# Performance work log

Measured on AMD Instinct MI355X. Metric: run time of the kernel, lower is better.

## Reference

```python
import jax, jax.numpy as jnp
import numpy as np

N_NODES = 100000
N_EDGES = 1600000
D_IN = 64
D_HID = 64
D_OUT = 64


def setup_inputs() -> dict:
    key = jax.random.key(0)
    ks = jax.random.split(key, 12)
    x = jax.random.normal(ks[0], (N_NODES, D_IN), dtype=jnp.float32)
    edge_index = jax.random.randint(ks[1], (2, N_EDGES), 0, N_NODES, dtype=jnp.int64)
    batch = jnp.zeros((N_NODES,), dtype=jnp.int64)
    # Glorot-ish init for GCNConv weights; PyG stores weight as [in, out] applied as x @ W.
    def lin(k, din, dout):
        s = 1.0 / np.sqrt(din)
        return jax.random.uniform(k, (din, dout), minval=-s, maxval=s, dtype=jnp.float32)
    W1 = lin(ks[2], D_IN, D_HID);  b1 = jnp.zeros((D_HID,), jnp.float32)
    W2 = lin(ks[3], D_HID, D_HID); b2 = jnp.zeros((D_HID,), jnp.float32)
    W3 = lin(ks[4], D_HID, D_HID); b3 = jnp.zeros((D_HID,), jnp.float32)
    W4 = lin(ks[5], D_HID, D_OUT); b4 = jnp.zeros((D_OUT,), jnp.float32)
    return {"x": x, "edge_index": edge_index, "batch": batch,
            "W1": W1, "b1": b1, "W2": W2, "b2": b2,
            "W3": W3, "b3": b3, "W4": W4, "b4": b4}


def reference(x, edge_index, batch, W1, b1, W2, b2, W3, b3, W4, b4):
    N = x.shape[0]
    loops = jnp.arange(N, dtype=edge_index.dtype)
    src = jnp.concatenate([edge_index[0], loops])  # [E+N]
    dst = jnp.concatenate([edge_index[1], loops])  # [E+N]
    # Symmetric normalization: deg over A + I (in-degree at dst), norm_e = d_src^-1/2 * d_dst^-1/2
    deg = jax.ops.segment_sum(jnp.ones(src.shape, dtype=x.dtype), dst, num_segments=N)
    dis = jnp.where(deg > 0, jax.lax.rsqrt(deg), 0.0)
    norm = (dis[src] * dis[dst])[:, None]  # [E+N, 1]

    def conv(h, W, b):
        h = h @ W                                   # [N, dout]
        msg = h[src] * norm                         # gather + scale, [E+N, dout]
        return jax.ops.segment_sum(msg, dst, num_segments=N) + b

    h = jax.nn.elu(conv(x, W1, b1))   # dropout_p=0.0 -> identity
    h = jax.nn.elu(conv(h, W2, b2))
    h = jax.nn.elu(conv(h, W3, b3))
    return conv(h, W4, b4)
```

## Files before the change

### kernel.cpp

```cpp
#include <hip/hip_runtime.h>

#define NN 100000
#define NE 1600000
#define DD 64
#define BSH 9
#define BSZ 512
#define NBKT 196
#define BCAP 16384
#define CHUNK 8192
#define NCH ((NE + CHUNK - 1) / CHUNK)
#define CSR2_CAP (NE + 16 * NN + 1024)


__global__ void k_zero(int* __restrict__ bcur, int* __restrict__ gcur,
                       float* __restrict__ h2sA, float* __restrict__ h2sB) {
    int t = threadIdx.x;
    if (t < NBKT) bcur[t] = 0;
    if (t == 255) *gcur = 0;
    if (t < DD) h2sA[(size_t)NN * DD + t] = 0.f;
    if (t >= 64 && t < 128) h2sB[(size_t)NN * DD + (t - 64)] = 0.f;
}


__global__ __launch_bounds__(256) void k_bscat(const int* __restrict__ ei,
                                               int* __restrict__ bcur,
                                               int* __restrict__ bkt) {
    __shared__ int h[NBKT], rbase[NBKT], rcur[NBKT];
    int t = threadIdx.x;
    for (int i = t; i < NBKT; i += 256) h[i] = 0;
    __syncthreads();
    int cb = blockIdx.x * CHUNK;
    int s[32], d[32];
#pragma unroll
    for (int i = 0; i < 32; ++i) {
        int e = cb + t + 256 * i;
        if (e < NE) {
            s[i] = ei[e];
            d[i] = ei[NE + e];
            atomicAdd(&h[d[i] >> BSH], 1);
        } else {
            d[i] = -1;
        }
    }
    __syncthreads();
    for (int i = t; i < NBKT; i += 256) {
        int c = h[i];
        rbase[i] = c ? atomicAdd(&bcur[i], c) : 0;
        rcur[i] = 0;
    }
    __syncthreads();
#pragma unroll
    for (int i = 0; i < 32; ++i) {
        if (d[i] >= 0) {
            int b = d[i] >> BSH;
            int pos = rbase[b] + atomicAdd(&rcur[b], 1);
            bkt[(size_t)b * BCAP + pos] = s[i] | ((d[i] & (BSZ - 1)) << 17);
        }
    }
}


__global__ __launch_bounds__(256) void k_merge(const int* __restrict__ bcur,
                                               const int* __restrict__ bkt,
                                               int* __restrict__ gcur,
                                               int* __restrict__ rbeg,
                                               int* __restrict__ rlen,
                                               double* __restrict__ dis,
                                               int* __restrict__ csr2) {
    __shared__ int cnt[BSZ];
    __shared__ int cur[BSZ];
    __shared__ int s2[256];
    __shared__ int sbase;
    int b = blockIdx.x, t = threadIdx.x;
    cnt[t] = 0; cnt[t + 256] = 0;
    __syncthreads();
    int ec = bcur[b];
    const int* row = bkt + (size_t)b * BCAP;
    for (int j = t; j < ec; j += 256)
        atomicAdd(&cnt[row[j] >> 17], 1);
    __syncthreads();
    int nb = b * BSZ;
    int n0 = nb + 2 * t, n1 = nb + 2 * t + 1;
    int c0 = (n0 < NN) ? cnt[2 * t] : -1;
    int c1 = (n1 < NN) ? cnt[2 * t + 1] : -1;
    int q0 = (c0 >= 0) ? ((c0 + 16) & ~15) : 0;
    int q1 = (c1 >= 0) ? ((c1 + 16) & ~15) : 0;
    s2[t] = q0 + q1;
    __syncthreads();
    for (int o = 1; o < 256; o <<= 1) {
        int v = (t >= o) ? s2[t - o] : 0;
        __syncthreads();
        s2[t] += v;
        __syncthreads();
    }
    if (t == 255) sbase = atomicAdd(gcur, s2[255]);
    __syncthreads();
    int base = sbase;
    int ex = s2[t] - (q0 + q1);
    if (c0 >= 0) {
        rbeg[n0] = base + ex; rlen[n0] = q0;
        dis[n0] = 1.0 / sqrt((double)(c0 + 1));
        csr2[base + ex] = n0;
        cur[2 * t] = ex + 1;
    }
    if (c1 >= 0) {
        rbeg[n1] = base + ex + q0; rlen[n1] = q1;
        dis[n1] = 1.0 / sqrt((double)(c1 + 1));
        csr2[base + ex + q0] = n1;
        cur[2 * t + 1] = ex + q0 + 1;
    }
    __syncthreads();
    for (int j = t; j < ec; j += 256) {
        int pk = row[j];
        int pos = base + atomicAdd(&cur[pk >> 17], 1);
        csr2[pos] = pk & 0x1FFFF;
    }
    __syncthreads();
    if (c0 >= 0) { int e0 = ex + q0;      for (int j = cur[2 * t];     j < e0; ++j) csr2[base + j] = NN; }
    if (c1 >= 0) { int e1 = ex + q0 + q1; for (int j = cur[2 * t + 1]; j < e1; ++j) csr2[base + j] = NN; }
}


__global__ __launch_bounds__(256) void k_gemm(const float* __restrict__ in,
                                              const float* __restrict__ W,
                                              const double* __restrict__ dis,
                                              float* __restrict__ h2s) {
    __shared__ float sW[DD * DD];
    __shared__ float sIn[128 * 65];
    int t = threadIdx.x;
    int brow = blockIdx.x * 128;
#pragma unroll
    for (int i = 0; i < 16; ++i) sW[t + 256 * i] = W[t + 256 * i];
#pragma unroll
    for (int i = 0; i < 32; ++i) {
        int idx = t + 256 * i;
        int rr = idx >> 6, kk = idx & 63;
        int gr = brow + rr; if (gr >= NN) gr = NN - 1;
        sIn[rr * 65 + kk] = in[(size_t)gr * DD + kk];
    }
    __syncthreads();
    int cg = t & 7;
    int rg = t >> 3;
    const float* sInB = &sIn[rg * 4 * 65];

    float aE[4][8], aO[4][8];
#pragma unroll
    for (int i = 0; i < 4; ++i)
#pragma unroll
        for (int j = 0; j < 8; ++j) { aE[i][j] = 0.f; aO[i][j] = 0.f; }

#pragma unroll 4
    for (int k = 0; k < DD; k += 2) {
        float4 w0 = *(const float4*)&sW[k * DD + cg * 8];
        float4 w1 = *(const float4*)&sW[k * DD + cg * 8 + 4];
        float4 w2 = *(const float4*)&sW[(k + 1) * DD + cg * 8];
        float4 w3 = *(const float4*)&sW[(k + 1) * DD + cg * 8 + 4];
        float wv0[8] = {w0.x, w0.y, w0.z, w0.w, w1.x, w1.y, w1.z, w1.w};
        float wv1[8] = {w2.x, w2.y, w2.z, w2.w, w3.x, w3.y, w3.z, w3.w};
#pragma unroll
        for (int i = 0; i < 4; ++i) {
            float a0 = sInB[i * 65 + k];
            float a1 = sInB[i * 65 + k + 1];
#pragma unroll
            for (int j = 0; j < 8; ++j) {
                aE[i][j] = fmaf(a0, wv0[j], aE[i][j]);
                aO[i][j] = fmaf(a1, wv1[j], aO[i][j]);
            }
        }
    }

#pragma unroll
    for (int i = 0; i < 4; ++i) {
        int row = brow + rg * 4 + i;
        if (row < NN) {
            double dr = dis[row];
            float o[8];
#pragma unroll
            for (int j = 0; j < 8; ++j)
                o[j] = (float)((double)(aE[i][j] + aO[i][j]) * dr);
            *(float4*)&h2s[(size_t)row * DD + cg * 8]     = make_float4(o[0], o[1], o[2], o[3]);
            *(float4*)&h2s[(size_t)row * DD + cg * 8 + 4] = make_float4(o[4], o[5], o[6], o[7]);
        }
    }
}


__global__ __launch_bounds__(256) void k_fag(const int* __restrict__ rbeg,
                                             const int* __restrict__ rlen,
                                             const int* __restrict__ csr2,
                                             const float* __restrict__ h2s_old,
                                             const double* __restrict__ dis,
                                             const float* __restrict__ bias,
                                             const float* __restrict__ W,
                                             float* __restrict__ h2s_new) {
    int t = threadIdx.x;
    int lane = t & 63;
    float wk[64];
#pragma unroll
    for (int k = 0; k < 64; ++k) wk[k] = W[k * DD + lane];
    float bv = bias[lane];
    int wglob = blockIdx.x * 4 + (t >> 6);
    int nwaves = gridDim.x * 4;
    for (int node = wglob; node < NN; node += nwaves) {
        int beg = __builtin_amdgcn_readfirstlane(rbeg[node]);
        int end = beg + __builtin_amdgcn_readfirstlane(rlen[node]);
        double a0 = 0.0, a1 = 0.0, a2 = 0.0, a3 = 0.0;
        for (int j = beg; j < end; j += 8) {
            int4 i0 = *(const int4*)&csr2[j];
            int4 i1 = *(const int4*)&csr2[j + 4];
            float v0 = h2s_old[(size_t)(unsigned)i0.x * DD + lane];
            float v1 = h2s_old[(size_t)(unsigned)i0.y * DD + lane];
            float v2 = h2s_old[(size_t)(unsigned)i0.z * DD + lane];
            float v3 = h2s_old[(size_t)(unsigned)i0.w * DD + lane];
            float v4 = h2s_old[(size_t)(unsigned)i1.x * DD + lane];
            float v5 = h2s_old[(size_t)(unsigned)i1.y * DD + lane];
            float v6 = h2s_old[(size_t)(unsigned)i1.z * DD + lane];
            float v7 = h2s_old[(size_t)(unsigned)i1.w * DD + lane];
            a0 += (double)v0; a1 += (double)v1;
            a2 += (double)v2; a3 += (double)v3;
            a0 += (double)v4; a1 += (double)v5;
            a2 += (double)v6; a3 += (double)v7;
        }
        double dn = dis[node];
        float vf = (float)(dn * ((a0 + a1) + (a2 + a3)) + (double)bv);
        if (vf <= 0.f) vf = expm1f(vf);
        int vb = __float_as_int(vf);
        float accE = 0.f, accO = 0.f;
#pragma unroll
        for (int k = 0; k < 64; k += 2) {
            float h0 = __int_as_float(__builtin_amdgcn_readlane(vb, k));
            float h1 = __int_as_float(__builtin_amdgcn_readlane(vb, k + 1));
            accE = fmaf(h0, wk[k], accE);
            accO = fmaf(h1, wk[k + 1], accO);
        }
        h2s_new[(size_t)node * DD + lane] = (float)((double)(accE + accO) * dn);
    }
}


__global__ __launch_bounds__(256) void k_aggr(const int* __restrict__ rbeg,
                                              const int* __restrict__ rlen,
                                              const int* __restrict__ csr2,
                                              const float* __restrict__ h2s,
                                              const double* __restrict__ dis,
                                              const float* __restrict__ b,
                                              float* __restrict__ out) {
    int gid = blockIdx.x * 256 + threadIdx.x;
    int node = gid >> 6;
    int lane = gid & 63;
    int beg = __builtin_amdgcn_readfirstlane(rbeg[node]);
    int end = beg + __builtin_amdgcn_readfirstlane(rlen[node]);
    double a0 = 0.0, a1 = 0.0, a2 = 0.0, a3 = 0.0;
    for (int j = beg; j < end; j += 16) {
        int4 i0 = *(const int4*)&csr2[j];
        int4 i1 = *(const int4*)&csr2[j + 4];
        int4 i2 = *(const int4*)&csr2[j + 8];
        int4 i3 = *(const int4*)&csr2[j + 12];
        float v0  = h2s[(size_t)(unsigned)i0.x * DD + lane];
        float v1  = h2s[(size_t)(unsigned)i0.y * DD + lane];
        float v2  = h2s[(size_t)(unsigned)i0.z * DD + lane];
        float v3  = h2s[(size_t)(unsigned)i0.w * DD + lane];
        float v4  = h2s[(size_t)(unsigned)i1.x * DD + lane];
        float v5  = h2s[(size_t)(unsigned)i1.y * DD + lane];
        float v6  = h2s[(size_t)(unsigned)i1.z * DD + lane];
        float v7  = h2s[(size_t)(unsigned)i1.w * DD + lane];
        float v8  = h2s[(size_t)(unsigned)i2.x * DD + lane];
        float v9  = h2s[(size_t)(unsigned)i2.y * DD + lane];
        float v10 = h2s[(size_t)(unsigned)i2.z * DD + lane];
        float v11 = h2s[(size_t)(unsigned)i2.w * DD + lane];
        float v12 = h2s[(size_t)(unsigned)i3.x * DD + lane];
        float v13 = h2s[(size_t)(unsigned)i3.y * DD + lane];
        float v14 = h2s[(size_t)(unsigned)i3.z * DD + lane];
        float v15 = h2s[(size_t)(unsigned)i3.w * DD + lane];
        a0 += (double)v0;  a1 += (double)v1;  a2 += (double)v2;  a3 += (double)v3;
        a0 += (double)v4;  a1 += (double)v5;  a2 += (double)v6;  a3 += (double)v7;
        a0 += (double)v8;  a1 += (double)v9;  a2 += (double)v10; a3 += (double)v11;
        a0 += (double)v12; a1 += (double)v13; a2 += (double)v14; a3 += (double)v15;
    }
    double sum = (a0 + a1) + (a2 + a3);
    out[gid] = (float)(dis[node] * sum + (double)b[lane]);
}


static inline size_t align256(size_t x) { return (x + 255) & ~(size_t)255; }

extern "C" void kernel_launch(void* const* d_in, const int* in_sizes, int n_in,
                              void* d_out, int out_size, void* d_ws, size_t ws_size,
                              hipStream_t stream) {
    const float* x  = (const float*)d_in[0];
    const int*   ei = (const int*)d_in[1];
    const float* W1 = (const float*)d_in[3];
    const float* b1 = (const float*)d_in[4];
    const float* W2 = (const float*)d_in[5];
    const float* b2 = (const float*)d_in[6];
    const float* W3 = (const float*)d_in[7];
    const float* b3 = (const float*)d_in[8];
    const float* W4 = (const float*)d_in[9];
    const float* b4 = (const float*)d_in[10];
    float* out = (float*)d_out;

    char* ws = (char*)d_ws;
    size_t off = 0;
    float*  h2sA = (float*) (ws + off); off = align256(off + (size_t)(NN + 1) * DD * sizeof(float));
    float*  h2sB = (float*) (ws + off); off = align256(off + (size_t)(NN + 1) * DD * sizeof(float));
    double* dis  = (double*)(ws + off); off = align256(off + (size_t)NN * sizeof(double));
    int*    rbeg = (int*)   (ws + off); off = align256(off + (size_t)NN * sizeof(int));
    int*    rlen = (int*)   (ws + off); off = align256(off + (size_t)NN * sizeof(int));
    int*    bcur = (int*)   (ws + off); off = align256(off + (size_t)(NBKT + 1) * sizeof(int));
    int*    gcur = (int*)   (ws + off); off = align256(off + 256 * sizeof(int));
    int*    bkt  = (int*)   (ws + off); off = align256(off + (size_t)NBKT * BCAP * sizeof(int));
    int*    csr2 = (int*)   (ws + off); off = align256(off + (size_t)CSR2_CAP * sizeof(int));

    k_zero <<<1, 256, 0, stream>>>(bcur, gcur, h2sA, h2sB);
    k_bscat<<<NCH, 256, 0, stream>>>(ei, bcur, bkt);
    k_merge<<<NBKT, 256, 0, stream>>>(bcur, bkt, gcur, rbeg, rlen, dis, csr2);

    const int NGB = (NN + 127) / 128;
    k_gemm<<<NGB, 256, 0, stream>>>(x, W1, dis, h2sA);
    k_fag <<<2048, 256, 0, stream>>>(rbeg, rlen, csr2, h2sA, dis, b1, W2, h2sB);
    k_fag <<<2048, 256, 0, stream>>>(rbeg, rlen, csr2, h2sB, dis, b2, W3, h2sA);
    k_fag <<<2048, 256, 0, stream>>>(rbeg, rlen, csr2, h2sA, dis, b3, W4, h2sB);
    k_aggr<<<NN / 4, 256, 0, stream>>>(rbeg, rlen, csr2, h2sB, dis, b4, out);
}
```

Baseline: 378.2 us.

## Replace fused aggregate-GEMM kernels with separate GEMM and aggregation per layer

Removes the fused k_fag kernel, which aggregated, applied ELU and did the next layer's matvec via readlane. Each layer now runs a tiled k_gemm followed by k_aggr, which gains an optional ELU flag, with intermediates ping-ponging between a workspace buffer and the output. This drops the per-node serial 64-step readlane matvec and the 64 weight registers per lane, which likely hurt occupancy. The cost is three extra launches and an extra full read and write of node features per layer.

```diff
diff --git a/kernel.cpp b/kernel.cpp
--- a/kernel.cpp
+++ b/kernel.cpp
@@ -13,12 +13,11 @@
 
 
 __global__ void k_zero(int* __restrict__ bcur, int* __restrict__ gcur,
-                       float* __restrict__ h2sA, float* __restrict__ h2sB) {
+                       float* __restrict__ h2s) {
     int t = threadIdx.x;
     if (t < NBKT) bcur[t] = 0;
     if (t == 255) *gcur = 0;
-    if (t < DD) h2sA[(size_t)NN * DD + t] = 0.f;
-    if (t >= 64 && t < 128) h2sB[(size_t)NN * DD + (t - 64)] = 0.f;
+    if (t < DD) h2s[(size_t)NN * DD + t] = 0.f;
 }
 
 
@@ -185,66 +184,14 @@
 }
 
 
-__global__ __launch_bounds__(256) void k_fag(const int* __restrict__ rbeg,
-                                             const int* __restrict__ rlen,
-                                             const int* __restrict__ csr2,
-                                             const float* __restrict__ h2s_old,
-                                             const double* __restrict__ dis,
-                                             const float* __restrict__ bias,
-                                             const float* __restrict__ W,
-                                             float* __restrict__ h2s_new) {
-    int t = threadIdx.x;
-    int lane = t & 63;
-    float wk[64];
-#pragma unroll
-    for (int k = 0; k < 64; ++k) wk[k] = W[k * DD + lane];
-    float bv = bias[lane];
-    int wglob = blockIdx.x * 4 + (t >> 6);
-    int nwaves = gridDim.x * 4;
-    for (int node = wglob; node < NN; node += nwaves) {
-        int beg = __builtin_amdgcn_readfirstlane(rbeg[node]);
-        int end = beg + __builtin_amdgcn_readfirstlane(rlen[node]);
-        double a0 = 0.0, a1 = 0.0, a2 = 0.0, a3 = 0.0;
-        for (int j = beg; j < end; j += 8) {
-            int4 i0 = *(const int4*)&csr2[j];
-            int4 i1 = *(const int4*)&csr2[j + 4];
-            float v0 = h2s_old[(size_t)(unsigned)i0.x * DD + lane];
-            float v1 = h2s_old[(size_t)(unsigned)i0.y * DD + lane];
-            float v2 = h2s_old[(size_t)(unsigned)i0.z * DD + lane];
-            float v3 = h2s_old[(size_t)(unsigned)i0.w * DD + lane];
-            float v4 = h2s_old[(size_t)(unsigned)i1.x * DD + lane];
-            float v5 = h2s_old[(size_t)(unsigned)i1.y * DD + lane];
-            float v6 = h2s_old[(size_t)(unsigned)i1.z * DD + lane];
-            float v7 = h2s_old[(size_t)(unsigned)i1.w * DD + lane];
-            a0 += (double)v0; a1 += (double)v1;
-            a2 += (double)v2; a3 += (double)v3;
-            a0 += (double)v4; a1 += (double)v5;
-            a2 += (double)v6; a3 += (double)v7;
-        }
-        double dn = dis[node];
-        float vf = (float)(dn * ((a0 + a1) + (a2 + a3)) + (double)bv);
-        if (vf <= 0.f) vf = expm1f(vf);
-        int vb = __float_as_int(vf);
-        float accE = 0.f, accO = 0.f;
-#pragma unroll
-        for (int k = 0; k < 64; k += 2) {
-            float h0 = __int_as_float(__builtin_amdgcn_readlane(vb, k));
-            float h1 = __int_as_float(__builtin_amdgcn_readlane(vb, k + 1));
-            accE = fmaf(h0, wk[k], accE);
-            accO = fmaf(h1, wk[k + 1], accO);
-        }
-        h2s_new[(size_t)node * DD + lane] = (float)((double)(accE + accO) * dn);
-    }
-}
-
-
 __global__ __launch_bounds__(256) void k_aggr(const int* __restrict__ rbeg,
                                               const int* __restrict__ rlen,
                                               const int* __restrict__ csr2,
                                               const float* __restrict__ h2s,
                                               const double* __restrict__ dis,
                                               const float* __restrict__ b,
-                                              float* __restrict__ out) {
+                                              float* __restrict__ out,
+                                              int apply_elu) {
     int gid = blockIdx.x * 256 + threadIdx.x;
     int node = gid >> 6;
     int lane = gid & 63;
@@ -278,7 +225,9 @@
         a0 += (double)v12; a1 += (double)v13; a2 += (double)v14; a3 += (double)v15;
     }
     double sum = (a0 + a1) + (a2 + a3);
-    out[gid] = (float)(dis[node] * sum + (double)b[lane]);
+    float vf = (float)(dis[node] * sum + (double)b[lane]);
+    if (apply_elu && vf <= 0.f) vf = expm1f(vf);
+    out[gid] = vf;
 }
 
 
@@ -301,8 +250,8 @@
 
     char* ws = (char*)d_ws;
     size_t off = 0;
-    float*  h2sA = (float*) (ws + off); off = align256(off + (size_t)(NN + 1) * DD * sizeof(float));
-    float*  h2sB = (float*) (ws + off); off = align256(off + (size_t)(NN + 1) * DD * sizeof(float));
+    float*  h2s  = (float*) (ws + off); off = align256(off + (size_t)(NN + 1) * DD * sizeof(float));
+    float*  A    = (float*) (ws + off); off = align256(off + (size_t)NN * DD * sizeof(float));
     double* dis  = (double*)(ws + off); off = align256(off + (size_t)NN * sizeof(double));
     int*    rbeg = (int*)   (ws + off); off = align256(off + (size_t)NN * sizeof(int));
     int*    rlen = (int*)   (ws + off); off = align256(off + (size_t)NN * sizeof(int));
@@ -311,14 +260,22 @@
     int*    bkt  = (int*)   (ws + off); off = align256(off + (size_t)NBKT * BCAP * sizeof(int));
     int*    csr2 = (int*)   (ws + off); off = align256(off + (size_t)CSR2_CAP * sizeof(int));
 
-    k_zero <<<1, 256, 0, stream>>>(bcur, gcur, h2sA, h2sB);
+    k_zero <<<1, 256, 0, stream>>>(bcur, gcur, h2s);
     k_bscat<<<NCH, 256, 0, stream>>>(ei, bcur, bkt);
     k_merge<<<NBKT, 256, 0, stream>>>(bcur, bkt, gcur, rbeg, rlen, dis, csr2);
 
+    struct Layer { const float* in; const float* W; const float* b; float* o; int elu; };
+    Layer L[4] = {
+        { x,   W1, b1, A,   1 },
+        { A,   W2, b2, out, 1 },
+        { out, W3, b3, A,   1 },
+        { A,   W4, b4, out, 0 },
+    };
+
     const int NGB = (NN + 127) / 128;
-    k_gemm<<<NGB, 256, 0, stream>>>(x, W1, dis, h2sA);
-    k_fag <<<2048, 256, 0, stream>>>(rbeg, rlen, csr2, h2sA, dis, b1, W2, h2sB);
-    k_fag <<<2048, 256, 0, stream>>>(rbeg, rlen, csr2, h2sB, dis, b2, W3, h2sA);
-    k_fag <<<2048, 256, 0, stream>>>(rbeg, rlen, csr2, h2sA, dis, b3, W4, h2sB);
-    k_aggr<<<NN / 4, 256, 0, stream>>>(rbeg, rlen, csr2, h2sB, dis, b4, out);
-}
+    for (int l = 0; l < 4; ++l) {
+        k_gemm<<<NGB, 256, 0, stream>>>(L[l].in, L[l].W, dis, h2s);
+        k_aggr<<<NN / 4, 256, 0, stream>>>(rbeg, rlen, csr2, h2s, dis,
+                                           L[l].b, L[l].o, L[l].elu);
+    }
+}
```

After: 370.3 us (median of 2 runs). -2.1%, faster.
